# Kernel tuning notes

Measured on AMD Instinct MI355X. Metric: run time of the kernel, lower is better.

## Reference

```python
import jax, jax.numpy as jnp
import numpy as np

B, S, D, K = 32, 512, 512, 2048
NHEADS, NHASH, HLEN = 8, 4, 16
COMMIT = 0.25


def _conv1d(x, w, b):
    # x: [B, C, S], w: [O, I, k] (torch Conv1d layout), 'same' padding for odd k
    k = w.shape[-1]
    y = jax.lax.conv_general_dilated(x, w, (1,), [(k // 2, k // 2)],
                                     dimension_numbers=('NCH', 'OIH', 'NCH'))
    return y + b[None, :, None]


def _mha(x, in_w, in_b, out_w, out_b, nheads):
    # torch nn.MultiheadAttention (batch_first) with packed in_proj
    b, s, d = x.shape
    dh = d // nheads
    qkv = x @ in_w.T + in_b
    q, k, v = jnp.split(qkv, 3, axis=-1)
    sp = lambda t: t.reshape(b, s, nheads, dh).transpose(0, 2, 1, 3)
    q, k, v = sp(q), sp(k), sp(v)
    attn = jax.nn.softmax(jnp.einsum('bhqd,bhkd->bhqk', q, k) * (dh ** -0.5), axis=-1)
    o = jnp.einsum('bhqk,bhkd->bhqd', attn, v).transpose(0, 2, 1, 3).reshape(b, s, d)
    return o @ out_w.T + out_b


def setup_inputs() -> dict:
    key = jax.random.key(0)
    ks = jax.random.split(key, 16)
    w = lambda k, shape, s=0.02: jax.random.normal(k, shape, jnp.float32) * s
    z = lambda *shape: jnp.zeros(shape, jnp.float32)
    return {
        'market_data': jax.random.normal(ks[0], (B, S, D), jnp.float32),
        'W_in': w(ks[1], (D, D)), 'b_in': z(D),
        'pos_enc': w(ks[2], (S, D)),
        'conv3_w': w(ks[3], (D, D, 3)), 'conv3_b': z(D),
        'conv5_w': w(ks[4], (D, D, 5)), 'conv5_b': z(D),
        'conv7_w': w(ks[5], (D, D, 7)), 'conv7_b': z(D),
        'conv9_w': w(ks[6], (D, D, 9)), 'conv9_b': z(D),
        'ms_proj_w': w(ks[7], (D, 4 * D)), 'ms_proj_b': z(D),
        'in_proj_w': w(ks[8], (3 * D, D)), 'in_proj_b': z(3 * D),
        'attn_out_w': w(ks[9], (D, D)), 'attn_out_b': z(D),
        'codebook': jax.random.uniform(ks[10], (K, D), jnp.float32, -1.0 / K, 1.0 / K),
        'hash_w': w(ks[11], (NHASH, HLEN, D), 1.0),
        'reg1_w': w(ks[12], (D // 2, D)), 'reg1_b': z(D // 2),
        'reg2_w': w(ks[13], (K, D // 2)), 'reg2_b': z(K),
    }


def reference(market_data, W_in, b_in, pos_enc, conv3_w, conv3_b, conv5_w, conv5_b,
              conv7_w, conv7_b, conv9_w, conv9_b, ms_proj_w, ms_proj_b,
              in_proj_w, in_proj_b, attn_out_w, attn_out_b, codebook, hash_w,
              reg1_w, reg1_b, reg2_w, reg2_b):
    # input projection
    x = market_data @ W_in.T + b_in                                   # [B,S,D]
    # --- subsequence encoder ---
    xp = x + pos_enc[:x.shape[1]][None]
    xt = xp.transpose(0, 2, 1)                                        # [B,D,S]
    scales = [jax.nn.relu(_conv1d(xt, cw, cb)).transpose(0, 2, 1)
              for cw, cb in ((conv3_w, conv3_b), (conv5_w, conv5_b),
                             (conv7_w, conv7_b), (conv9_w, conv9_b))]
    multi = jnp.concatenate(scales, axis=-1)                          # [B,S,4D]
    proj = multi @ ms_proj_w.T + ms_proj_b                            # [B,S,D]
    enc = proj + _mha(proj, in_proj_w, in_proj_b, attn_out_w, attn_out_b, NHEADS)
    # --- vector quantizer (eval mode: no EMA update) ---
    flat = enc.reshape(-1, D)                                         # [N,D]
    dist = (jnp.sum(flat * flat, axis=1, keepdims=True)
            + jnp.sum(codebook * codebook, axis=1)
            - 2.0 * (flat @ codebook.T))                              # [N,K]
    idx = jnp.argmin(dist, axis=1)                                    # [N]
    quant = codebook[idx].reshape(enc.shape)
    commit = jnp.mean((jax.lax.stop_gradient(quant) - enc) ** 2)
    cb_loss = jnp.mean((quant - jax.lax.stop_gradient(enc)) ** 2)
    vq_loss = COMMIT * commit + cb_loss
    quant_st = enc + jax.lax.stop_gradient(quant - enc)               # straight-through
    # --- hash encoder on semantic ids ---
    hash_codes = (jnp.einsum('bsd,nhd->bsnh', quant_st, hash_w) > 0).astype(jnp.float32)
    # --- regime classifier ---
    h = jax.nn.relu(quant_st @ reg1_w.T + reg1_b)
    regime = jax.nn.softmax(h @ reg2_w.T + reg2_b, axis=-1)
    return (quant_st, vq_loss, idx.reshape(enc.shape[:-1]), hash_codes, regime)
```

## Files before the change

kernel.cpp:

```cpp
#include <hip/hip_runtime.h>
#include <hip/hip_bf16.h>


#define GF_BIAS 1
#define GF_RELU 2
#define GF_ADD  4
#define GF_POS  8
#define GF_ACC  16

typedef _Float16 f16x8 __attribute__((ext_vector_type(8)));
typedef float    f32x4 __attribute__((ext_vector_type(4)));

static constexpr long long O_QUANT = 0LL;
static constexpr long long O_LOSS  = 8388608LL;
static constexpr long long O_IDX   = 8388609LL;
static constexpr long long O_HASH  = 8404993LL;
static constexpr long long O_REG   = 9453569LL;
static constexpr long long O_END   = 43008001LL;

static constexpr long long W_XP    = 0LL;
static constexpr long long W_CT    = 8388608LL;
static constexpr long long W_PROJ  = 16777216LL;
static constexpr long long W_VW    = 25165824LL;
static constexpr long long W_HREG  = 33554432LL;
static constexpr long long W_T     = 34078720LL;
static constexpr long long W_IDX   = 34209792LL;
static constexpr long long W_ASUM  = 34226176LL;
static constexpr long long W_CBB   = 34258944LL;
static constexpr long long W_LPART = 34263040LL;
static constexpr long long W_PBV   = 34271232LL;
static constexpr long long W_PBI   = 34336768LL;
static constexpr long long W_END   = 34402304LL;

__device__ __forceinline__ unsigned int pack_hl(float x)
{
    _Float16 h = (_Float16)x;
    float hf = (float)h;
    _Float16 l = (_Float16)(x - hf);
    unsigned short hb = __builtin_bit_cast(unsigned short, h);
    unsigned short lb = __builtin_bit_cast(unsigned short, l);
    return (unsigned int)hb | ((unsigned int)lb << 16);
}

__device__ __forceinline__ void split2(float x, unsigned short& h, unsigned short& l)
{
    _Float16 hf = (_Float16)x;
    _Float16 lf = (_Float16)(x - (float)hf);
    h = __builtin_bit_cast(unsigned short, hf);
    l = __builtin_bit_cast(unsigned short, lf);
}

__device__ __forceinline__ float unpack_sum(unsigned int u)
{
    _Float16 h = __builtin_bit_cast(_Float16, (unsigned short)(u & 0xffff));
    _Float16 l = __builtin_bit_cast(_Float16, (unsigned short)(u >> 16));
    return (float)h + (float)l;
}

__global__ __launch_bounds__(256)
void split_inplace_r21(float* __restrict__ p)
{
    long long i = (long long)blockIdx.x*256 + threadIdx.x;
    float x = p[i];
    ((unsigned int*)p)[i] = pack_hl(x);
}

__global__ __launch_bounds__(256)
void split_cb_r21(const float* __restrict__ cb, unsigned int* __restrict__ cbhl)
{
    long long i = (long long)blockIdx.x*256 + threadIdx.x;
    cbhl[i] = pack_hl(cb[i] * 2048.0f);
}

template<int KT>
__global__ __launch_bounds__(256)
void conv_w_tr_r21(const float* __restrict__ w, unsigned int* __restrict__ wt)
{
    long long i = (long long)blockIdx.x*256 + threadIdx.x;
    int o  = (int)(i / (512*KT));
    int rem= (int)(i % (512*KT));
    int t  = rem >> 9;
    int ii = rem & 511;
    wt[i] = pack_hl(w[(long long)o*512*KT + (long long)ii*KT + t]);
}

template<int KT>
__global__ __launch_bounds__(256)
void conv_mfma_r21(const unsigned int* __restrict__ xphl,
                   const unsigned int* __restrict__ wthl,
                   const float* __restrict__ bias, float* __restrict__ outp)
{
    constexpr int PAD = KT / 2;
    __shared__ unsigned short Ah[136][40];
    __shared__ unsigned short Al[136][40];
    __shared__ unsigned short Bh[128][40];
    __shared__ unsigned short Bl[128][40];
    const int tid  = threadIdx.x;
    const int lane = tid & 63;
    const int wave = tid >> 6;
    const int wm = (wave >> 1) * 64, wn = (wave & 1) * 64;
    const int bm = blockIdx.x * 128, bn = blockIdx.y * 128;
    const int l15 = lane & 15;
    const int lk8 = (lane >> 4) * 8;
    const int rbase = (lane >> 4) * 4;
    const int sb = bm & 511;
    const int brow0 = tid >> 3, bc = tid & 7;

    f32x4 acc[4][4];
    #pragma unroll
    for (int i=0;i<4;i++)
        #pragma unroll
        for (int j=0;j<4;j++)
            acc[i][j] = (f32x4){0.f,0.f,0.f,0.f};

    for (int i0 = 0; i0 < 512; i0 += 32) {
        __syncthreads();
        for (int sl = tid; sl < 136*8; sl += 256) {
            const int row = sl >> 3, c = sl & 7;
            const int srow = sb + row - 4;
            uint4 v = make_uint4(0u,0u,0u,0u);
            if (srow >= 0 && srow < 512)
                v = *(const uint4*)(xphl + (long long)(bm + row - 4)*512 + i0 + c*4);
            Ah[row][c*4+0] = (unsigned short)(v.x & 0xffff);
            Ah[row][c*4+1] = (unsigned short)(v.y & 0xffff);
            Ah[row][c*4+2] = (unsigned short)(v.z & 0xffff);
            Ah[row][c*4+3] = (unsigned short)(v.w & 0xffff);
            Al[row][c*4+0] = (unsigned short)(v.x >> 16);
            Al[row][c*4+1] = (unsigned short)(v.y >> 16);
            Al[row][c*4+2] = (unsigned short)(v.z >> 16);
            Al[row][c*4+3] = (unsigned short)(v.w >> 16);
        }
        uint4 vb[4];
        #pragma unroll
        for (int q = 0; q < 4; ++q) {
            const int row = brow0 + q*32;
            vb[q] = *(const uint4*)(wthl + (long long)(bn + row)*(KT*512) + 0*512 + i0 + bc*4);
        }
        for (int t = 0; t < KT; ++t) {
            #pragma unroll
            for (int q = 0; q < 4; ++q) {
                const int row = brow0 + q*32;
                Bh[row][bc*4+0] = (unsigned short)(vb[q].x & 0xffff);
                Bh[row][bc*4+1] = (unsigned short)(vb[q].y & 0xffff);
                Bh[row][bc*4+2] = (unsigned short)(vb[q].z & 0xffff);
                Bh[row][bc*4+3] = (unsigned short)(vb[q].w & 0xffff);
                Bl[row][bc*4+0] = (unsigned short)(vb[q].x >> 16);
                Bl[row][bc*4+1] = (unsigned short)(vb[q].y >> 16);
                Bl[row][bc*4+2] = (unsigned short)(vb[q].z >> 16);
                Bl[row][bc*4+3] = (unsigned short)(vb[q].w >> 16);
            }
            if (t + 1 < KT) {
                #pragma unroll
                for (int q = 0; q < 4; ++q) {
                    const int row = brow0 + q*32;
                    vb[q] = *(const uint4*)(wthl + (long long)(bn + row)*(KT*512) + (t+1)*512 + i0 + bc*4);
                }
            }
            __syncthreads();
            const int tofs = t - PAD + 4;
            f16x8 ah[4], al[4], bh[4], bl[4];
            #pragma unroll
            for (int mi = 0; mi < 4; ++mi) {
                ah[mi] = *(const f16x8*)(&Ah[wm + mi*16 + l15 + tofs][lk8]);
                al[mi] = *(const f16x8*)(&Al[wm + mi*16 + l15 + tofs][lk8]);
            }
            #pragma unroll
            for (int nj = 0; nj < 4; ++nj) {
                bh[nj] = *(const f16x8*)(&Bh[wn + nj*16 + l15][lk8]);
                bl[nj] = *(const f16x8*)(&Bl[wn + nj*16 + l15][lk8]);
            }
            #pragma unroll
            for (int mi = 0; mi < 4; ++mi)
                #pragma unroll
                for (int nj = 0; nj < 4; ++nj) {
                    acc[mi][nj] = __builtin_amdgcn_mfma_f32_16x16x32_f16(ah[mi], bh[nj], acc[mi][nj], 0, 0, 0);
                    acc[mi][nj] = __builtin_amdgcn_mfma_f32_16x16x32_f16(ah[mi], bl[nj], acc[mi][nj], 0, 0, 0);
                    acc[mi][nj] = __builtin_amdgcn_mfma_f32_16x16x32_f16(al[mi], bh[nj], acc[mi][nj], 0, 0, 0);
                }
            if (t + 1 < KT) __syncthreads();
        }
    }
    #pragma unroll
    for (int mi = 0; mi < 4; ++mi) {
        #pragma unroll
        for (int nj = 0; nj < 4; ++nj) {
            const int col = bn + wn + nj*16 + l15;
            const float bcol = bias[col];
            #pragma unroll
            for (int r = 0; r < 4; ++r) {
                const int row = bm + wm + mi*16 + rbase + r;
                float v = acc[mi][nj][r] + bcol;
                outp[(long long)row*512 + col] = fmaxf(v, 0.0f);
            }
        }
    }
}

template<int FLAGS>
__global__ __launch_bounds__(256)
void gemm_mfma_r21(const float* __restrict__ A, const float* __restrict__ Bm,
                   const float* __restrict__ bias, const float* __restrict__ pos,
                   const float* __restrict__ addsrc, float* __restrict__ C,
                   int Kdim, int lda, int ldb, int ldc)
{
    __shared__ unsigned short Ah[128][56];
    __shared__ unsigned short Al[128][56];
    __shared__ unsigned short Bh[128][56];
    __shared__ unsigned short Bl[128][56];
    const int tid  = threadIdx.x;
    const int lane = tid & 63;
    const int wave = tid >> 6;
    const int wm = (wave >> 1) * 64, wn = (wave & 1) * 64;
    const int bm = blockIdx.x * 128, bn = blockIdx.y * 128;
    const int l15 = lane & 15;
    const int lk8 = (lane >> 4) * 8;
    const int rbase = (lane >> 4) * 4;
    const int cg   = tid & 7;
    const int rw0  = tid >> 3;

    f32x4 acc[4][4];
    #pragma unroll
    for (int i=0;i<4;i++)
        #pragma unroll
        for (int j=0;j<4;j++)
            acc[i][j] = (f32x4){0.f,0.f,0.f,0.f};

    for (int k0 = 0; k0 < Kdim; k0 += 32) {
        float4 fa[4], fb[4];
        #pragma unroll
        for (int q = 0; q < 4; ++q) {
            const int row = rw0 + q*32;
            fa[q] = *(const float4*)(A  + (long long)(bm + row)*lda + k0 + cg*4);
            fb[q] = *(const float4*)(Bm + (long long)(bn + row)*ldb + k0 + cg*4);
        }
        __syncthreads();
        #pragma unroll
        for (int q = 0; q < 4; ++q) {
            const int row = rw0 + q*32;
            ushort4 ah_, al_, bh_, bl_;
            split2(fa[q].x, ah_.x, al_.x);
            split2(fa[q].y, ah_.y, al_.y);
            split2(fa[q].z, ah_.z, al_.z);
            split2(fa[q].w, ah_.w, al_.w);
            split2(fb[q].x, bh_.x, bl_.x);
            split2(fb[q].y, bh_.y, bl_.y);
            split2(fb[q].z, bh_.z, bl_.z);
            split2(fb[q].w, bh_.w, bl_.w);
            *(ushort4*)(&Ah[row][cg*4]) = ah_;
            *(ushort4*)(&Al[row][cg*4]) = al_;
            *(ushort4*)(&Bh[row][cg*4]) = bh_;
            *(ushort4*)(&Bl[row][cg*4]) = bl_;
        }
        __syncthreads();
        f16x8 ah[4], al[4], bh[4], bl[4];
        #pragma unroll
        for (int mi = 0; mi < 4; ++mi) {
            ah[mi] = *(const f16x8*)(&Ah[wm + mi*16 + l15][lk8]);
            al[mi] = *(const f16x8*)(&Al[wm + mi*16 + l15][lk8]);
        }
        #pragma unroll
        for (int nj = 0; nj < 4; ++nj) {
            bh[nj] = *(const f16x8*)(&Bh[wn + nj*16 + l15][lk8]);
            bl[nj] = *(const f16x8*)(&Bl[wn + nj*16 + l15][lk8]);
        }
        #pragma unroll
        for (int mi = 0; mi < 4; ++mi)
            #pragma unroll
            for (int nj = 0; nj < 4; ++nj) {
                acc[mi][nj] = __builtin_amdgcn_mfma_f32_16x16x32_f16(ah[mi], bh[nj], acc[mi][nj], 0, 0, 0);
                acc[mi][nj] = __builtin_amdgcn_mfma_f32_16x16x32_f16(ah[mi], bl[nj], acc[mi][nj], 0, 0, 0);
                acc[mi][nj] = __builtin_amdgcn_mfma_f32_16x16x32_f16(al[mi], bh[nj], acc[mi][nj], 0, 0, 0);
            }
    }
    #pragma unroll
    for (int mi = 0; mi < 4; ++mi) {
        #pragma unroll
        for (int nj = 0; nj < 4; ++nj) {
            const int col = bn + wn + nj*16 + l15;
            #pragma unroll
            for (int r = 0; r < 4; ++r) {
                const int row = bm + wm + mi*16 + rbase + r;
                float v = acc[mi][nj][r];
                if constexpr (FLAGS & GF_BIAS) v += bias[col];
                if constexpr (FLAGS & GF_POS)  v += pos[(long long)(row & 511)*512 + col];
                if constexpr (FLAGS & GF_ADD)  v += addsrc[(long long)row*ldc + col];
                if constexpr (FLAGS & GF_ACC)  v += C[(long long)row*ldc + col];
                if constexpr (FLAGS & GF_RELU) v = fmaxf(v, 0.0f);
                C[(long long)row*ldc + col] = v;
            }
        }
    }
}

__global__ __launch_bounds__(256)
void attn_mfma_r21(const float* __restrict__ Qbuf, const float* __restrict__ Kbuf,
                   const float* __restrict__ Vbuf, float* __restrict__ att)
{
    __shared__ unsigned short Qh[64][68];
    __shared__ unsigned short Ql[64][68];
    __shared__ unsigned short Kh[64][68];
    __shared__ unsigned short Kl[64][68];
    __shared__ unsigned short Vh[64][68];
    __shared__ unsigned short Vl[64][68];
    const int tid  = threadIdx.x;
    const int lane = tid & 63;
    const int wave = tid >> 6;
    const int l15  = lane & 15;
    const int lq   = lane >> 4;
    const int lq8  = lq * 8;
    const int bid = blockIdx.x;
    const int qt = bid & 7, h = (bid >> 3) & 7, b = bid >> 6;
    const int row0 = b*512 + qt*64;

    #pragma unroll
    for (int u = 0; u < 16; ++u) {
        int e = u*256 + tid;
        int r = e >> 6, c = e & 63;
        float q = Qbuf[(long long)(row0 + r)*512 + h*64 + c] * 0.125f;
        unsigned short hs, ls;
        split2(q, hs, ls);
        Qh[r][c] = hs; Ql[r][c] = ls;
    }

    float m[4], l[4];
    f32x4 accO[4];
    #pragma unroll
    for (int r=0;r<4;r++){ m[r] = -1e30f; l[r] = 0.f; }
    #pragma unroll
    for (int j=0;j<4;j++) accO[j] = (f32x4){0.f,0.f,0.f,0.f};

    for (int kv = 0; kv < 512; kv += 64) {
        __syncthreads();
        #pragma unroll
        for (int u = 0; u < 16; ++u) {
            int e = u*256 + tid;
            int r = e >> 6, c = e & 63;
            float kvf = Kbuf[(long long)(b*512 + kv + r)*512 + h*64 + c];
            float vvf = Vbuf[(long long)(b*512 + kv + r)*512 + h*64 + c];
            unsigned short hs, ls;
            split2(kvf, hs, ls);
            Kh[r][c] = hs; Kl[r][c] = ls;
            split2(vvf, hs, ls);
            Vh[c][r] = hs; Vl[c][r] = ls;
        }
        __syncthreads();
        f32x4 accS[4];
        #pragma unroll
        for (int j=0;j<4;j++) accS[j] = (f32x4){0.f,0.f,0.f,0.f};
        #pragma unroll
        for (int ks = 0; ks < 2; ++ks) {
            f16x8 qh = *(const f16x8*)(&Qh[wave*16 + l15][ks*32 + lq8]);
            f16x8 ql = *(const f16x8*)(&Ql[wave*16 + l15][ks*32 + lq8]);
            #pragma unroll
            for (int nj = 0; nj < 4; ++nj) {
                f16x8 kh = *(const f16x8*)(&Kh[nj*16 + l15][ks*32 + lq8]);
                f16x8 kl = *(const f16x8*)(&Kl[nj*16 + l15][ks*32 + lq8]);
                accS[nj] = __builtin_amdgcn_mfma_f32_16x16x32_f16(qh, kh, accS[nj], 0, 0, 0);
                accS[nj] = __builtin_amdgcn_mfma_f32_16x16x32_f16(qh, kl, accS[nj], 0, 0, 0);
                accS[nj] = __builtin_amdgcn_mfma_f32_16x16x32_f16(ql, kh, accS[nj], 0, 0, 0);
            }
        }
        #pragma unroll
        for (int r = 0; r < 4; ++r) {
            float tm = fmaxf(fmaxf(accS[0][r], accS[1][r]), fmaxf(accS[2][r], accS[3][r]));
            #pragma unroll
            for (int msk = 1; msk < 16; msk <<= 1) tm = fmaxf(tm, __shfl_xor(tm, msk, 64));
            float mn = fmaxf(m[r], tm);
            float scale = expf(m[r] - mn);
            float rs = 0.f;
            #pragma unroll
            for (int nj = 0; nj < 4; ++nj) {
                float p = expf(accS[nj][r] - mn);
                accS[nj][r] = p;
                rs += p;
            }
            #pragma unroll
            for (int msk = 1; msk < 16; msk <<= 1) rs += __shfl_xor(rs, msk, 64);
            l[r] = l[r]*scale + rs;
            m[r] = mn;
            #pragma unroll
            for (int nj = 0; nj < 4; ++nj) accO[nj][r] *= scale;
        }
        __syncthreads();
        #pragma unroll
        for (int r = 0; r < 4; ++r)
            #pragma unroll
            for (int nj = 0; nj < 4; ++nj) {
                unsigned short hs, ls;
                split2(accS[nj][r], hs, ls);
                Kh[wave*16 + lq*4 + r][nj*16 + l15] = hs;
                Kl[wave*16 + lq*4 + r][nj*16 + l15] = ls;
            }
        __syncthreads();
        #pragma unroll
        for (int ks = 0; ks < 2; ++ks) {
            f16x8 ph = *(const f16x8*)(&Kh[wave*16 + l15][ks*32 + lq8]);
            f16x8 pl = *(const f16x8*)(&Kl[wave*16 + l15][ks*32 + lq8]);
            #pragma unroll
            for (int nj = 0; nj < 4; ++nj) {
                f16x8 vh = *(const f16x8*)(&Vh[nj*16 + l15][ks*32 + lq8]);
                f16x8 vl = *(const f16x8*)(&Vl[nj*16 + l15][ks*32 + lq8]);
                accO[nj] = __builtin_amdgcn_mfma_f32_16x16x32_f16(ph, vh, accO[nj], 0, 0, 0);
                accO[nj] = __builtin_amdgcn_mfma_f32_16x16x32_f16(ph, vl, accO[nj], 0, 0, 0);
                accO[nj] = __builtin_amdgcn_mfma_f32_16x16x32_f16(pl, vh, accO[nj], 0, 0, 0);
            }
        }
    }
    #pragma unroll
    for (int nj = 0; nj < 4; ++nj)
        #pragma unroll
        for (int r = 0; r < 4; ++r) {
            const int row = row0 + wave*16 + lq*4 + r;
            att[(long long)row*512 + h*64 + nj*16 + l15] = accO[nj][r] / l[r];
        }
}

__global__ __launch_bounds__(256)
void row_sumsq_r21(const float* __restrict__ X, double* __restrict__ outp)
{
    const int row  = blockIdx.x*4 + (threadIdx.x >> 6);
    const int lane = threadIdx.x & 63;
    double s = 0.0;
    #pragma unroll
    for (int u = 0; u < 8; ++u) {
        float v = X[(long long)row*512 + lane + u*64];
        s += (double)v * (double)v;
    }
    #pragma unroll
    for (int msk = 32; msk; msk >>= 1) s += __shfl_xor(s, msk, 64);
    if (lane == 0) outp[row] = s;
}

__global__ __launch_bounds__(256)
void vq_argmin_mfma_r21(const unsigned int* __restrict__ enchl,
                        const unsigned int* __restrict__ cbhl,
                        const double* __restrict__ Asum, const double* __restrict__ cbB,
                        float* __restrict__ pbv, int* __restrict__ pbi)
{
    __shared__ unsigned int smem[10240];
    unsigned short* AhP = (unsigned short*)smem;
    unsigned short* AlP = AhP + 128*40;
    unsigned short* BhP = AlP + 128*40;
    unsigned short* BlP = BhP + 128*40;
    float* bvsP = (float*)smem;
    int*   bisP = (int*)(smem + 4096);

    const int tid  = threadIdx.x;
    const int lane = tid & 63;
    const int wave = tid >> 6;
    const int wm = (wave >> 1) * 64, wn = (wave & 1) * 64;
    const int bm = blockIdx.x * 128;
    const int l15 = lane & 15;
    const int lk8 = (lane >> 4) * 8;
    const int rbase = (lane >> 4) * 4;
    const int cg   = tid & 7;
    const int rw0  = tid >> 3;

    float bestv[16]; int besti[16];
    #pragma unroll
    for (int g = 0; g < 16; ++g) { bestv[g] = 3.0e38f; besti[g] = 2048; }

    for (int nb = 0; nb < 4; ++nb) {
        const int ct0 = blockIdx.y * 512 + nb * 128;
        f32x4 acc[4][4];
        #pragma unroll
        for (int i=0;i<4;i++)
            #pragma unroll
            for (int j=0;j<4;j++)
                acc[i][j] = (f32x4){0.f,0.f,0.f,0.f};

        for (int k0 = 0; k0 < 512; k0 += 32) {
            uint4 va[4], vb[4];
            #pragma unroll
            for (int q = 0; q < 4; ++q) {
                const int row = rw0 + q*32;
                va[q] = *(const uint4*)(enchl + (long long)(bm + row)*512 + k0 + cg*4);
                vb[q] = *(const uint4*)(cbhl  + (long long)(ct0 + row)*512 + k0 + cg*4);
            }
            __syncthreads();
            #pragma unroll
            for (int q = 0; q < 4; ++q) {
                const int row = rw0 + q*32;
                AhP[row*40 + cg*4+0] = (unsigned short)(va[q].x & 0xffff);
                AhP[row*40 + cg*4+1] = (unsigned short)(va[q].y & 0xffff);
                AhP[row*40 + cg*4+2] = (unsigned short)(va[q].z & 0xffff);
                AhP[row*40 + cg*4+3] = (unsigned short)(va[q].w & 0xffff);
                AlP[row*40 + cg*4+0] = (unsigned short)(va[q].x >> 16);
// ... 25 lines not shown
            for (int mi = 0; mi < 4; ++mi)
                #pragma unroll
                for (int nj = 0; nj < 4; ++nj) {
                    acc[mi][nj] = __builtin_amdgcn_mfma_f32_16x16x32_f16(ah[mi], bh[nj], acc[mi][nj], 0, 0, 0);
                    acc[mi][nj] = __builtin_amdgcn_mfma_f32_16x16x32_f16(ah[mi], bl[nj], acc[mi][nj], 0, 0, 0);
                    acc[mi][nj] = __builtin_amdgcn_mfma_f32_16x16x32_f16(al[mi], bh[nj], acc[mi][nj], 0, 0, 0);
                }
        }
        #pragma unroll
        for (int mi = 0; mi < 4; ++mi) {
            #pragma unroll
            for (int r = 0; r < 4; ++r) {
                const int g = mi*4 + r;
                const float anf = (float)Asum[bm + wm + mi*16 + rbase + r];
                #pragma unroll
                for (int nj = 0; nj < 4; ++nj) {
                    const int col = ct0 + wn + nj*16 + l15;
                    const float bf = (float)cbB[col];
                    const float s1 = anf + bf;
                    const float dot = acc[mi][nj][r] * (1.0f/2048.0f);
                    const float df  = 2.0f * dot;
                    const float qd  = s1 - df;
                    if (qd < bestv[g] || (qd == bestv[g] && col < besti[g])) {
                        bestv[g] = qd; besti[g] = col;
                    }
                }
            }
        }
    }
    __syncthreads();
    #pragma unroll
    for (int mi = 0; mi < 4; ++mi)
        #pragma unroll
        for (int r = 0; r < 4; ++r) {
            const int row  = wm + mi*16 + rbase + r;
            const int slot = (wave & 1)*16 + l15;
            bvsP[row*32 + slot] = bestv[mi*4 + r];
            bisP[row*32 + slot] = besti[mi*4 + r];
        }
    __syncthreads();
    if (tid < 128) {
        float bv = bvsP[tid*32]; int bi = bisP[tid*32];
        #pragma unroll
        for (int s = 1; s < 32; ++s) {
            float v = bvsP[tid*32 + s]; int ii = bisP[tid*32 + s];
            if (v < bv || (v == bv && ii < bi)) { bv = v; bi = ii; }
        }
        pbv[(long long)blockIdx.y*16384 + bm + tid] = bv;
        pbi[(long long)blockIdx.y*16384 + bm + tid] = bi;
    }
}

__global__ __launch_bounds__(256)
void vq_reduce_r21(const float* __restrict__ pbv, const int* __restrict__ pbi,
                   int* __restrict__ idxout, float* __restrict__ out)
{
    int n = blockIdx.x*256 + threadIdx.x;
    if (n >= 16384) return;
    float bv = pbv[n]; int bi = pbi[n];
    #pragma unroll
    for (int q = 1; q < 4; ++q) {
        float v = pbv[q*16384 + n]; int ii = pbi[q*16384 + n];
        if (v < bv || (v == bv && ii < bi)) { bv = v; bi = ii; }
    }
    int ci = bi & 2047;
    idxout[n] = ci;
    out[O_IDX + n] = (float)ci;
}

__global__ __launch_bounds__(256)
void vq_loss_partial_r21(const unsigned int* __restrict__ enchl,
                         const float* __restrict__ cb,
                         const int* __restrict__ idxp, double* __restrict__ part)
{
    __shared__ double red[4];
    const int row  = blockIdx.x*4 + (threadIdx.x >> 6);
    const int lane = threadIdx.x & 63;
    const int ci = idxp[row] & 2047;
    double s = 0.0;
    #pragma unroll
    for (int u = 0; u < 8; ++u) {
        int d = lane + u*64;
        float e = unpack_sum(enchl[(long long)row*512 + d]);
        double dv = (double)cb[(long long)ci*512 + d] - (double)e;
        s += dv * dv;
    }
    #pragma unroll
    for (int msk = 32; msk; msk >>= 1) s += __shfl_xor(s, msk, 64);
    if (lane == 0) red[threadIdx.x >> 6] = s;
    __syncthreads();
    if (threadIdx.x == 0)
        part[blockIdx.x] = red[0] + red[1] + red[2] + red[3];
}

template<int FLAGS>
__global__ __launch_bounds__(256)
void gemm_bt_r21(const float* __restrict__ A, const float* __restrict__ Bm,
                 const float* __restrict__ bias, const float* __restrict__ pos,
                 const float* __restrict__ addsrc, float* __restrict__ C,
                 int Kdim, int lda, int ldb, int ldc)
{
    __shared__ float As[16][132];
    __shared__ float Bs[16][132];
    const int tid = threadIdx.x;
    const int tx = tid & 15, ty = tid >> 4;
    const int bm = blockIdx.x * 128, bn = blockIdx.y * 128;
    const int r0 = tid >> 2;
    const int kg = (tid & 3) << 2;
    const float* Arow0 = A  + (long long)(bm + r0) * lda + kg;
    const float* Arow1 = A  + (long long)(bm + r0 + 64) * lda + kg;
    const float* Brow0 = Bm + (long long)(bn + r0) * ldb + kg;
    const float* Brow1 = Bm + (long long)(bn + r0 + 64) * ldb + kg;

    float acc[8][8] = {};
    for (int k0 = 0; k0 < Kdim; k0 += 16) {
        float4 a0 = *(const float4*)(Arow0 + k0);
        float4 a1 = *(const float4*)(Arow1 + k0);
        float4 b0 = *(const float4*)(Brow0 + k0);
        float4 b1 = *(const float4*)(Brow1 + k0);
        __syncthreads();
        As[kg+0][r0]=a0.x; As[kg+1][r0]=a0.y; As[kg+2][r0]=a0.z; As[kg+3][r0]=a0.w;
        As[kg+0][r0+64]=a1.x; As[kg+1][r0+64]=a1.y; As[kg+2][r0+64]=a1.z; As[kg+3][r0+64]=a1.w;
        Bs[kg+0][r0]=b0.x; Bs[kg+1][r0]=b0.y; Bs[kg+2][r0]=b0.z; Bs[kg+3][r0]=b0.w;
        Bs[kg+0][r0+64]=b1.x; Bs[kg+1][r0+64]=b1.y; Bs[kg+2][r0+64]=b1.z; Bs[kg+3][r0+64]=b1.w;
        __syncthreads();
        #pragma unroll
        for (int kk = 0; kk < 16; ++kk) {
            float a[8], b[8];
            #pragma unroll
            for (int i=0;i<8;i++) a[i] = As[kk][ty*8+i];
            #pragma unroll
            for (int j=0;j<4;j++) b[j]   = Bs[kk][tx*4+j];
            #pragma unroll
            for (int j=0;j<4;j++) b[4+j] = Bs[kk][64+tx*4+j];
            #pragma unroll
            for (int i=0;i<8;i++)
                #pragma unroll
                for (int j=0;j<8;j++)
                    acc[i][j] = fmaf(a[i], b[j], acc[i][j]);
        }
    }
    #pragma unroll
    for (int i=0;i<8;i++){
        const int row = bm + ty*8 + i;
        #pragma unroll
        for (int j=0;j<8;j++){
            const int col = bn + ((j < 4) ? (tx*4 + j) : (64 + tx*4 + (j-4)));
            float v = acc[i][j];
            if constexpr (FLAGS & GF_BIAS) v += bias[col];
            if constexpr (FLAGS & GF_POS)  v += pos[(long long)(row & 511)*512 + col];
            if constexpr (FLAGS & GF_ADD)  v += addsrc[(long long)row*ldc + col];
            if constexpr (FLAGS & GF_ACC)  v += C[(long long)row*ldc + col];
            if constexpr (FLAGS & GF_RELU) v = fmaxf(v, 0.0f);
            C[(long long)row*ldc + col] = v;
        }
    }
}

__global__ __launch_bounds__(256)
void softmax_rows_r21(float* __restrict__ R)
{
    const int row = blockIdx.x;
    const int tid = threadIdx.x;
    __shared__ float  redf[256];
    __shared__ double redd[256];
    float* p = R + (long long)row * 2048;
    float mx = -1e30f;
    for (int c = tid; c < 2048; c += 256) mx = fmaxf(mx, p[c]);
    redf[tid] = mx; __syncthreads();
    for (int s2 = 128; s2; s2 >>= 1) { if (tid < s2) redf[tid] = fmaxf(redf[tid], redf[tid+s2]); __syncthreads(); }
    mx = redf[0];
    double sum = 0.0;
    for (int c = tid; c < 2048; c += 256) { float e = expf(p[c] - mx); p[c] = e; sum += e; }
    redd[tid] = sum; __syncthreads();
    for (int s2 = 128; s2; s2 >>= 1) { if (tid < s2) redd[tid] += redd[tid+s2]; __syncthreads(); }
    double tot = redd[0];
    for (int c = tid; c < 2048; c += 256) p[c] = (float)((double)p[c] / tot);
}

__global__ __launch_bounds__(256)
void hash_table_r21(const float* __restrict__ cb, const float* __restrict__ hw,
                    float* __restrict__ T)
{
    const int k = blockIdx.x*4 + (threadIdx.x >> 6);
    const int j = threadIdx.x & 63;
    double s = 0.0;
    for (int d = 0; d < 512; ++d)
        s += (double)cb[(long long)k*512 + d] * (double)hw[(long long)j*512 + d];
    T[(long long)k*64 + j] = (s > 0.0) ? 1.0f : 0.0f;
}

__global__ void write_loss_r21(const double* __restrict__ part,
                               float* __restrict__ out)
{
    __shared__ double red[256];
    double s = 0.0;
    for (int i = threadIdx.x; i < 4096; i += 256) s += part[i];
    red[threadIdx.x] = s; __syncthreads();
    for (int s2 = 128; s2; s2 >>= 1) {
        if (threadIdx.x < s2) red[threadIdx.x] += red[threadIdx.x + s2];
        __syncthreads();
    }
    if (threadIdx.x == 0)
        out[O_LOSS] = (float)(1.25 * red[0] / 8388608.0);
}

__global__ __launch_bounds__(256)
void write_regime_r21(const float* __restrict__ R, const int* __restrict__ idxp,
                      float* __restrict__ out)
{
    long long i = (long long)blockIdx.x*256 + threadIdx.x;
    if (i >= 33554432LL) return;
    int n = (int)(i >> 11), c = (int)(i & 2047);
    int ci = idxp[n] & 2047;
    out[O_REG + i] = R[(long long)ci*2048 + c];
}

__global__ __launch_bounds__(256)
void write_hash_r21(const float* __restrict__ T, const int* __restrict__ idxp,
                    float* __restrict__ out)
{
    long long i = (long long)blockIdx.x*256 + threadIdx.x;
    if (i >= 1048576LL) return;
    int n = (int)(i >> 6), j = (int)(i & 63);
    int ci = idxp[n] & 2047;
    out[O_HASH + i] = T[(long long)ci*64 + j];
}

__global__ __launch_bounds__(256)
void write_quant_r21(const float* __restrict__ cb, const int* __restrict__ idxp,
                     float* __restrict__ out)
{
    long long i = (long long)blockIdx.x*256 + threadIdx.x;
    if (i >= 8388608LL) return;
    int n = (int)(i >> 9), d = (int)(i & 511);
    int ci = idxp[n] & 2047;
    out[O_QUANT + i] = cb[(long long)ci*512 + d];
}

extern "C" void kernel_launch(void* const* d_in, const int* in_sizes, int n_in,
                              void* d_out, int out_size, void* d_ws, size_t ws_size,
                              hipStream_t stream)
{
    (void)in_sizes; (void)n_in; (void)out_size;
    const float* market = (const float*)d_in[0];
    const float* W_in   = (const float*)d_in[1];
    const float* b_in   = (const float*)d_in[2];
    const float* pos    = (const float*)d_in[3];
    const float* c3w = (const float*)d_in[4];  const float* c3b = (const float*)d_in[5];
    const float* c5w = (const float*)d_in[6];  const float* c5b = (const float*)d_in[7];
    const float* c7w = (const float*)d_in[8];  const float* c7b = (const float*)d_in[9];
    const float* c9w = (const float*)d_in[10]; const float* c9b = (const float*)d_in[11];
    const float* msw = (const float*)d_in[12]; const float* msb = (const float*)d_in[13];
    const float* inw = (const float*)d_in[14]; const float* inb = (const float*)d_in[15];
    const float* aow = (const float*)d_in[16]; const float* aob = (const float*)d_in[17];
    const float* cb  = (const float*)d_in[18]; const float* hw  = (const float*)d_in[19];
    const float* r1w = (const float*)d_in[20]; const float* r1b = (const float*)d_in[21];
    const float* r2w = (const float*)d_in[22]; const float* r2b = (const float*)d_in[23];

    if (ws_size < (size_t)W_END * sizeof(float)) return;

    float* ws    = (float*)d_ws;
    float* xp    = ws + W_XP;
    float* convt = ws + W_CT;
    float* projp = ws + W_PROJ;
    unsigned int* wt3 = (unsigned int*)(ws + W_VW);
    unsigned int* wt5 = wt3 + 512*512*3;
    unsigned int* wt7 = wt5 + 512*512*5;
    unsigned int* wt9 = wt7 + 512*512*7;
    float* Vbufp = ws + W_VW;
    float* hregp = ws + W_HREG;
    float* Tp    = ws + W_T;
    int*    idxp  = (int*)(ws + W_IDX);
    double* asump = (double*)(ws + W_ASUM);
    double* cbbp  = (double*)(ws + W_CBB);
    double* lpart = (double*)(ws + W_LPART);
    float*  pbvp  = ws + W_PBV;
    int*    pbip  = (int*)(ws + W_PBI);
    unsigned int* cbhl = (unsigned int*)(ws + W_PROJ + 4194304);

    float* out = (float*)d_out;

    float* Qbufp = xp;
    float* attp  = xp;
    float* Kbufp = convt;
    float* encp  = convt;
    float* Rp    = projp;

    const unsigned int* xpu  = (const unsigned int*)xp;
    const unsigned int* encu = (const unsigned int*)encp;

    conv_w_tr_r21<3><<<3072, 256, 0, stream>>>(c3w, wt3);
    conv_w_tr_r21<5><<<5120, 256, 0, stream>>>(c5w, wt5);
    conv_w_tr_r21<7><<<7168, 256, 0, stream>>>(c7w, wt7);
    conv_w_tr_r21<9><<<9216, 256, 0, stream>>>(c9w, wt9);

    const dim3 gT(128, 4);

    gemm_mfma_r21<GF_BIAS|GF_POS><<<gT, 256, 0, stream>>>(market, W_in, b_in, pos, nullptr, xp, 512, 512, 512, 512);
    split_inplace_r21<<<32768, 256, 0, stream>>>(xp);

    conv_mfma_r21<3><<<gT, 256, 0, stream>>>(xpu, wt3, c3b, convt);
    gemm_mfma_r21<GF_BIAS><<<gT, 256, 0, stream>>>(convt, msw + 0*512, msb, nullptr, nullptr, projp, 512, 512, 2048, 512);
    conv_mfma_r21<5><<<gT, 256, 0, stream>>>(xpu, wt5, c5b, convt);
    gemm_mfma_r21<GF_ACC><<<gT, 256, 0, stream>>>(convt, msw + 1*512, nullptr, nullptr, nullptr, projp, 512, 512, 2048, 512);
    conv_mfma_r21<7><<<gT, 256, 0, stream>>>(xpu, wt7, c7b, convt);
    gemm_mfma_r21<GF_ACC><<<gT, 256, 0, stream>>>(convt, msw + 2*512, nullptr, nullptr, nullptr, projp, 512, 512, 2048, 512);
    conv_mfma_r21<9><<<gT, 256, 0, stream>>>(xpu, wt9, c9b, convt);
    gemm_mfma_r21<GF_ACC><<<gT, 256, 0, stream>>>(convt, msw + 3*512, nullptr, nullptr, nullptr, projp, 512, 512, 2048, 512);

    gemm_mfma_r21<GF_BIAS><<<gT, 256, 0, stream>>>(projp, inw + 512*512,  inb + 512,  nullptr, nullptr, Kbufp, 512, 512, 512, 512);
    gemm_mfma_r21<GF_BIAS><<<gT, 256, 0, stream>>>(projp, inw + 1024*512, inb + 1024, nullptr, nullptr, Vbufp, 512, 512, 512, 512);
    gemm_mfma_r21<GF_BIAS><<<gT, 256, 0, stream>>>(projp, inw,            inb,        nullptr, nullptr, Qbufp, 512, 512, 512, 512);

    attn_mfma_r21<<<2048, 256, 0, stream>>>(Qbufp, Kbufp, Vbufp, attp);

    gemm_mfma_r21<GF_BIAS|GF_ADD><<<gT, 256, 0, stream>>>(attp, aow, aob, nullptr, projp, encp, 512, 512, 512, 512);

    row_sumsq_r21<<<4096, 256, 0, stream>>>(encp, asump);
    row_sumsq_r21<<<512,  256, 0, stream>>>(cb, cbbp);
    split_inplace_r21<<<32768, 256, 0, stream>>>(encp);
    split_cb_r21<<<4096, 256, 0, stream>>>(cb, cbhl);
    vq_argmin_mfma_r21<<<dim3(128, 4), 256, 0, stream>>>(encu, cbhl, asump, cbbp, pbvp, pbip);
    vq_reduce_r21<<<64, 256, 0, stream>>>(pbvp, pbip, idxp, out);
    vq_loss_partial_r21<<<4096, 256, 0, stream>>>(encu, cb, idxp, lpart);

    gemm_bt_r21<GF_BIAS|GF_RELU><<<dim3(16, 2),  256, 0, stream>>>(cb, r1w, r1b, nullptr, nullptr, hregp, 512, 512, 512, 256);
    gemm_bt_r21<GF_BIAS><<<dim3(16, 16), 256, 0, stream>>>(hregp, r2w, r2b, nullptr, nullptr, Rp, 256, 256, 256, 2048);
    softmax_rows_r21<<<2048, 256, 0, stream>>>(Rp);
    hash_table_r21<<<512, 256, 0, stream>>>(cb, hw, Tp);

    write_loss_r21<<<1, 256, 0, stream>>>(lpart, out);
    write_regime_r21<<<131072, 256, 0, stream>>>(Rp, idxp, out);
    write_hash_r21<<<4096, 256, 0, stream>>>(Tp, idxp, out);
    write_quant_r21<<<32768, 256, 0, stream>>>(cb, idxp, out);
}
```

Before: 1.554 ms.

## Keep activations in packed fp16 hi/lo format across all GEMMs and attention

Every GEMM, conv and attention kernel now reads and writes activations as a packed hi/lo fp16 pair instead of fp32. Weights and inputs are pre-split once, so the per-tile split2 conversion inside the GEMM and attention loaders goes away. The Q scale is folded into the Q projection epilogue, and the separate in-place split passes over xp and enc are dropped. This adds several weight-split launches, and accumulating through packed pairs could change rounding slightly.

```diff
diff --git a/kernel.cpp b/kernel.cpp
--- a/kernel.cpp
+++ b/kernel.cpp
@@ -4,9 +4,10 @@
 
 #define GF_BIAS 1
 #define GF_RELU 2
-#define GF_ADD  4
+#define GF_ADDP 4
 #define GF_POS  8
-#define GF_ACC  16
+#define GF_ACCP 16
+#define GF_QSCALE 32
 
 typedef _Float16 f16x8 __attribute__((ext_vector_type(8)));
 typedef float    f32x4 __attribute__((ext_vector_type(4)));
@@ -58,15 +59,14 @@
 }
 
 __global__ __launch_bounds__(256)
-void split_inplace_r21(float* __restrict__ p)
+void split_hl_r22(const float* __restrict__ src, unsigned int* __restrict__ dst)
 {
     long long i = (long long)blockIdx.x*256 + threadIdx.x;
-    float x = p[i];
-    ((unsigned int*)p)[i] = pack_hl(x);
-}
-
-__global__ __launch_bounds__(256)
-void split_cb_r21(const float* __restrict__ cb, unsigned int* __restrict__ cbhl)
+    dst[i] = pack_hl(src[i]);
+}
+
+__global__ __launch_bounds__(256)
+void split_cb_r22(const float* __restrict__ cb, unsigned int* __restrict__ cbhl)
 {
     long long i = (long long)blockIdx.x*256 + threadIdx.x;
     cbhl[i] = pack_hl(cb[i] * 2048.0f);
@@ -74,7 +74,7 @@
 
 template<int KT>
 __global__ __launch_bounds__(256)
-void conv_w_tr_r21(const float* __restrict__ w, unsigned int* __restrict__ wt)
+void conv_w_tr_r22(const float* __restrict__ w, unsigned int* __restrict__ wt)
 {
     long long i = (long long)blockIdx.x*256 + threadIdx.x;
     int o  = (int)(i / (512*KT));
@@ -86,9 +86,9 @@
 
 template<int KT>
 __global__ __launch_bounds__(256)
-void conv_mfma_r21(const unsigned int* __restrict__ xphl,
+void conv_mfma_r22(const unsigned int* __restrict__ xphl,
                    const unsigned int* __restrict__ wthl,
-                   const float* __restrict__ bias, float* __restrict__ outp)
+                   const float* __restrict__ bias, unsigned int* __restrict__ outp)
 {
     constexpr int PAD = KT / 2;
     __shared__ unsigned short Ah[136][40];
@@ -190,7 +190,7 @@
             for (int r = 0; r < 4; ++r) {
                 const int row = bm + wm + mi*16 + rbase + r;
                 float v = acc[mi][nj][r] + bcol;
-                outp[(long long)row*512 + col] = fmaxf(v, 0.0f);
+                outp[(long long)row*512 + col] = pack_hl(fmaxf(v, 0.0f));
             }
         }
     }
@@ -198,15 +198,15 @@
 
 template<int FLAGS>
 __global__ __launch_bounds__(256)
-void gemm_mfma_r21(const float* __restrict__ A, const float* __restrict__ Bm,
-                   const float* __restrict__ bias, const float* __restrict__ pos,
-                   const float* __restrict__ addsrc, float* __restrict__ C,
-                   int Kdim, int lda, int ldb, int ldc)
-{
-    __shared__ unsigned short Ah[128][56];
-    __shared__ unsigned short Al[128][56];
-    __shared__ unsigned short Bh[128][56];
-    __shared__ unsigned short Bl[128][56];
+void gemm_hl_r22(const unsigned int* __restrict__ A, const unsigned int* __restrict__ Bm,
+                 const float* __restrict__ bias, const float* __restrict__ pos,
+                 const unsigned int* __restrict__ addsrc, unsigned int* __restrict__ C,
+                 int Kdim, int lda, int ldb, int ldc)
+{
+    __shared__ unsigned short Ah[128][40];
+    __shared__ unsigned short Al[128][40];
+    __shared__ unsigned short Bh[128][40];
+    __shared__ unsigned short Bl[128][40];
     const int tid  = threadIdx.x;
     const int lane = tid & 63;
     const int wave = tid >> 6;
@@ -226,30 +226,33 @@
             acc[i][j] = (f32x4){0.f,0.f,0.f,0.f};
 
     for (int k0 = 0; k0 < Kdim; k0 += 32) {
-        float4 fa[4], fb[4];
+        uint4 va[4], vb[4];
         #pragma unroll
         for (int q = 0; q < 4; ++q) {
             const int row = rw0 + q*32;
-            fa[q] = *(const float4*)(A  + (long long)(bm + row)*lda + k0 + cg*4);
-            fb[q] = *(const float4*)(Bm + (long long)(bn + row)*ldb + k0 + cg*4);
+            va[q] = *(const uint4*)(A  + (long long)(bm + row)*lda + k0 + cg*4);
+            vb[q] = *(const uint4*)(Bm + (long long)(bn + row)*ldb + k0 + cg*4);
         }
         __syncthreads();
         #pragma unroll
         for (int q = 0; q < 4; ++q) {
             const int row = rw0 + q*32;
-            ushort4 ah_, al_, bh_, bl_;
-            split2(fa[q].x, ah_.x, al_.x);
-            split2(fa[q].y, ah_.y, al_.y);
-            split2(fa[q].z, ah_.z, al_.z);
-            split2(fa[q].w, ah_.w, al_.w);
-            split2(fb[q].x, bh_.x, bl_.x);
-            split2(fb[q].y, bh_.y, bl_.y);
-            split2(fb[q].z, bh_.z, bl_.z);
-            split2(fb[q].w, bh_.w, bl_.w);
-            *(ushort4*)(&Ah[row][cg*4]) = ah_;
-            *(ushort4*)(&Al[row][cg*4]) = al_;
-            *(ushort4*)(&Bh[row][cg*4]) = bh_;
-            *(ushort4*)(&Bl[row][cg*4]) = bl_;
+            Ah[row][cg*4+0] = (unsigned short)(va[q].x & 0xffff);
+            Ah[row][cg*4+1] = (unsigned short)(va[q].y & 0xffff);
+            Ah[row][cg*4+2] = (unsigned short)(va[q].z & 0xffff);
+            Ah[row][cg*4+3] = (unsigned short)(va[q].w & 0xffff);
+            Al[row][cg*4+0] = (unsigned short)(va[q].x >> 16);
+            Al[row][cg*4+1] = (unsigned short)(va[q].y >> 16);
+            Al[row][cg*4+2] = (unsigned short)(va[q].z >> 16);
+            Al[row][cg*4+3] = (unsigned short)(va[q].w >> 16);
+            Bh[row][cg*4+0] = (unsigned short)(vb[q].x & 0xffff);
+            Bh[row][cg*4+1] = (unsigned short)(vb[q].y & 0xffff);
+            Bh[row][cg*4+2] = (unsigned short)(vb[q].z & 0xffff);
+            Bh[row][cg*4+3] = (unsigned short)(vb[q].w & 0xffff);
+            Bl[row][cg*4+0] = (unsigned short)(vb[q].x >> 16);
+            Bl[row][cg*4+1] = (unsigned short)(vb[q].y >> 16);
+            Bl[row][cg*4+2] = (unsigned short)(vb[q].z >> 16);
+            Bl[row][cg*4+3] = (unsigned short)(vb[q].w >> 16);
         }
         __syncthreads();
         f16x8 ah[4], al[4], bh[4], bl[4];
@@ -283,18 +286,18 @@
                 float v = acc[mi][nj][r];
                 if constexpr (FLAGS & GF_BIAS) v += bias[col];
                 if constexpr (FLAGS & GF_POS)  v += pos[(long long)(row & 511)*512 + col];
-                if constexpr (FLAGS & GF_ADD)  v += addsrc[(long long)row*ldc + col];
-                if constexpr (FLAGS & GF_ACC)  v += C[(long long)row*ldc + col];
-                if constexpr (FLAGS & GF_RELU) v = fmaxf(v, 0.0f);
-                C[(long long)row*ldc + col] = v;
-            }
-        }
-    }
-}
-
-__global__ __launch_bounds__(256)
-void attn_mfma_r21(const float* __restrict__ Qbuf, const float* __restrict__ Kbuf,
-                   const float* __restrict__ Vbuf, float* __restrict__ att)
+                if constexpr (FLAGS & GF_ADDP) v += unpack_sum(addsrc[(long long)row*ldc + col]);
+                if constexpr (FLAGS & GF_ACCP) v += unpack_sum(C[(long long)row*ldc + col]);
+                if constexpr (FLAGS & GF_QSCALE) v *= 0.125f;
+                C[(long long)row*ldc + col] = pack_hl(v);
+            }
+        }
+    }
+}
+
+__global__ __launch_bounds__(256)
+void attn_mfma_r22(const unsigned int* __restrict__ Qbuf, const unsigned int* __restrict__ Kbuf,
+                   const unsigned int* __restrict__ Vbuf, unsigned int* __restrict__ att)
 {
     __shared__ unsigned short Qh[64][68];
     __shared__ unsigned short Ql[64][68];
@@ -316,10 +319,9 @@
     for (int u = 0; u < 16; ++u) {
         int e = u*256 + tid;
         int r = e >> 6, c = e & 63;
-        float q = Qbuf[(long long)(row0 + r)*512 + h*64 + c] * 0.125f;
-        unsigned short hs, ls;
-        split2(q, hs, ls);
-        Qh[r][c] = hs; Ql[r][c] = ls;
+        unsigned int uq = Qbuf[(long long)(row0 + r)*512 + h*64 + c];
+        Qh[r][c] = (unsigned short)(uq & 0xffff);
+        Ql[r][c] = (unsigned short)(uq >> 16);
     }
 
     float m[4], l[4];
@@ -335,13 +337,12 @@
         for (int u = 0; u < 16; ++u) {
             int e = u*256 + tid;
             int r = e >> 6, c = e & 63;
-            float kvf = Kbuf[(long long)(b*512 + kv + r)*512 + h*64 + c];
-            float vvf = Vbuf[(long long)(b*512 + kv + r)*512 + h*64 + c];
-            unsigned short hs, ls;
-            split2(kvf, hs, ls);
-            Kh[r][c] = hs; Kl[r][c] = ls;
-            split2(vvf, hs, ls);
-            Vh[c][r] = hs; Vl[c][r] = ls;
+            unsigned int uk = Kbuf[(long long)(b*512 + kv + r)*512 + h*64 + c];
+            unsigned int uv = Vbuf[(long long)(b*512 + kv + r)*512 + h*64 + c];
+            Kh[r][c] = (unsigned short)(uk & 0xffff);
+            Kl[r][c] = (unsigned short)(uk >> 16);
+            Vh[c][r] = (unsigned short)(uv & 0xffff);
+            Vl[c][r] = (unsigned short)(uv >> 16);
         }
         __syncthreads();
         f32x4 accS[4];
@@ -411,12 +412,12 @@
         #pragma unroll
         for (int r = 0; r < 4; ++r) {
             const int row = row0 + wave*16 + lq*4 + r;
-            att[(long long)row*512 + h*64 + nj*16 + l15] = accO[nj][r] / l[r];
-        }
-}
-
-__global__ __launch_bounds__(256)
-void row_sumsq_r21(const float* __restrict__ X, double* __restrict__ outp)
+            att[(long long)row*512 + h*64 + nj*16 + l15] = pack_hl(accO[nj][r] / l[r]);
+        }
+}
+
+__global__ __launch_bounds__(256)
+void row_sumsq_r22(const float* __restrict__ X, double* __restrict__ outp)
 {
     const int row  = blockIdx.x*4 + (threadIdx.x >> 6);
     const int lane = threadIdx.x & 63;
@@ -432,7 +433,23 @@
 }
 
 __global__ __launch_bounds__(256)
-void vq_argmin_mfma_r21(const unsigned int* __restrict__ enchl,
+void row_sumsq_hl_r22(const unsigned int* __restrict__ X, double* __restrict__ outp)
+{
+    const int row  = blockIdx.x*4 + (threadIdx.x >> 6);
+    const int lane = threadIdx.x & 63;
+    double s = 0.0;
+    #pragma unroll
+    for (int u = 0; u < 8; ++u) {
+        float v = unpack_sum(X[(long long)row*512 + lane + u*64]);
+        s += (double)v * (double)v;
+    }
+    #pragma unroll
+    for (int msk = 32; msk; msk >>= 1) s += __shfl_xor(s, msk, 64);
+    if (lane == 0) outp[row] = s;
+}
+
+__global__ __launch_bounds__(256)
+void vq_argmin_mfma_r22(const unsigned int* __restrict__ enchl,
                         const unsigned int* __restrict__ cbhl,
                         const double* __restrict__ Asum, const double* __restrict__ cbB,
                         float* __restrict__ pbv, int* __restrict__ pbi)
@@ -564,7 +581,7 @@
 }
 
 __global__ __launch_bounds__(256)
-void vq_reduce_r21(const float* __restrict__ pbv, const int* __restrict__ pbi,
+void vq_reduce_r22(const float* __restrict__ pbv, const int* __restrict__ pbi,
                    int* __restrict__ idxout, float* __restrict__ out)
 {
     int n = blockIdx.x*256 + threadIdx.x;
@@ -581,7 +598,7 @@
 }
 
 __global__ __launch_bounds__(256)
-void vq_loss_partial_r21(const unsigned int* __restrict__ enchl,
+void vq_loss_partial_r22(const unsigned int* __restrict__ enchl,
                          const float* __restrict__ cb,
                          const int* __restrict__ idxp, double* __restrict__ part)
 {
@@ -607,7 +624,7 @@
 
 template<int FLAGS>
 __global__ __launch_bounds__(256)
-void gemm_bt_r21(const float* __restrict__ A, const float* __restrict__ Bm,
+void gemm_bt_r22(const float* __restrict__ A, const float* __restrict__ Bm,
                  const float* __restrict__ bias, const float* __restrict__ pos,
                  const float* __restrict__ addsrc, float* __restrict__ C,
                  int Kdim, int lda, int ldb, int ldc)
@@ -660,9 +677,6 @@
             const int col = bn + ((j < 4) ? (tx*4 + j) : (64 + tx*4 + (j-4)));
             float v = acc[i][j];
             if constexpr (FLAGS & GF_BIAS) v += bias[col];
-            if constexpr (FLAGS & GF_POS)  v += pos[(long long)(row & 511)*512 + col];
-            if constexpr (FLAGS & GF_ADD)  v += addsrc[(long long)row*ldc + col];
-            if constexpr (FLAGS & GF_ACC)  v += C[(long long)row*ldc + col];
             if constexpr (FLAGS & GF_RELU) v = fmaxf(v, 0.0f);
             C[(long long)row*ldc + col] = v;
         }
@@ -670,7 +684,7 @@
 }
 
 __global__ __launch_bounds__(256)
-void softmax_rows_r21(float* __restrict__ R)
+void softmax_rows_r22(float* __restrict__ R)
 {
     const int row = blockIdx.x;
     const int tid = threadIdx.x;
@@ -691,7 +705,7 @@
 }
 
 __global__ __launch_bounds__(256)
-void hash_table_r21(const float* __restrict__ cb, const float* __restrict__ hw,
+void hash_table_r22(const float* __restrict__ cb, const float* __restrict__ hw,
                     float* __restrict__ T)
 {
     const int k = blockIdx.x*4 + (threadIdx.x >> 6);
@@ -702,7 +716,7 @@
     T[(long long)k*64 + j] = (s > 0.0) ? 1.0f : 0.0f;
 }
 
-__global__ void write_loss_r21(const double* __restrict__ part,
+__global__ void write_loss_r22(const double* __restrict__ part,
                                float* __restrict__ out)
 {
     __shared__ double red[256];
@@ -718,7 +732,7 @@
 }
 
 __global__ __launch_bounds__(256)
-void write_regime_r21(const float* __restrict__ R, const int* __restrict__ idxp,
+void write_regime_r22(const float* __restrict__ R, const int* __restrict__ idxp,
                       float* __restrict__ out)
 {
     long long i = (long long)blockIdx.x*256 + threadIdx.x;
@@ -729,7 +743,7 @@
 }
 
 __global__ __launch_bounds__(256)
-void write_hash_r21(const float* __restrict__ T, const int* __restrict__ idxp,
+void write_hash_r22(const float* __restrict__ T, const int* __restrict__ idxp,
                     float* __restrict__ out)
 {
     long long i = (long long)blockIdx.x*256 + threadIdx.x;
@@ -740,7 +754,7 @@
 }
 
 __global__ __launch_bounds__(256)
-void write_quant_r21(const float* __restrict__ cb, const int* __restrict__ idxp,
+void write_quant_r22(const float* __restrict__ cb, const int* __restrict__ idxp,
                      float* __restrict__ out)
 {
     long long i = (long long)blockIdx.x*256 + threadIdx.x;
@@ -772,15 +786,22 @@
 
     if (ws_size < (size_t)W_END * sizeof(float)) return;
 
-    float* ws    = (float*)d_ws;
-    float* xp    = ws + W_XP;
-    float* convt = ws + W_CT;
-    float* projp = ws + W_PROJ;
-    unsigned int* wt3 = (unsigned int*)(ws + W_VW);
+    float* ws = (float*)d_ws;
+    unsigned int* xphl   = (unsigned int*)(ws + W_XP);
+    unsigned int* cthl   = (unsigned int*)(ws + W_CT);
+    unsigned int* projhl = (unsigned int*)(ws + W_PROJ);
+    unsigned int* vwbase = (unsigned int*)(ws + W_VW);
+    unsigned int* wt3 = vwbase;
     unsigned int* wt5 = wt3 + 512*512*3;
     unsigned int* wt7 = wt5 + 512*512*5;
     unsigned int* wt9 = wt7 + 512*512*7;
-    float* Vbufp = ws + W_VW;
+    unsigned int* mswhl  = vwbase + 6291456;
+    unsigned int* winhl  = mswhl + 1048576;
+    unsigned int* inwqhl = winhl + 262144;
+    unsigned int* inwkhl = inwqhl + 262144;
+    unsigned int* vhl    = vwbase;
+    unsigned int* inwvhl = (unsigned int*)(ws + W_HREG);
+    unsigned int* aowhl  = inwvhl + 262144;
     float* hregp = ws + W_HREG;
     float* Tp    = ws + W_T;
     int*    idxp  = (int*)(ws + W_IDX);
@@ -790,60 +811,57 @@
     float*  pbvp  = ws + W_PBV;
     int*    pbip  = (int*)(ws + W_PBI);
     unsigned int* cbhl = (unsigned int*)(ws + W_PROJ + 4194304);
+    float* Rp = ws + W_PROJ;
 
     float* out = (float*)d_out;
 
-    float* Qbufp = xp;
-    float* attp  = xp;
-    float* Kbufp = convt;
-    float* encp  = convt;
-    float* Rp    = projp;
-
-    const unsigned int* xpu  = (const unsigned int*)xp;
-    const unsigned int* encu = (const unsigned int*)encp;
-
-    conv_w_tr_r21<3><<<3072, 256, 0, stream>>>(c3w, wt3);
-    conv_w_tr_r21<5><<<5120, 256, 0, stream>>>(c5w, wt5);
-    conv_w_tr_r21<7><<<7168, 256, 0, stream>>>(c7w, wt7);
-    conv_w_tr_r21<9><<<9216, 256, 0, stream>>>(c9w, wt9);
+    conv_w_tr_r22<3><<<3072, 256, 0, stream>>>(c3w, wt3);
+    conv_w_tr_r22<5><<<5120, 256, 0, stream>>>(c5w, wt5);
+    conv_w_tr_r22<7><<<7168, 256, 0, stream>>>(c7w, wt7);
+    conv_w_tr_r22<9><<<9216, 256, 0, stream>>>(c9w, wt9);
+    split_hl_r22<<<32768, 256, 0, stream>>>(market, cthl);
+    split_hl_r22<<<1024,  256, 0, stream>>>(W_in, winhl);
+    split_hl_r22<<<4096,  256, 0, stream>>>(msw, mswhl);
+    split_hl_r22<<<1024,  256, 0, stream>>>(inw,            inwqhl);
+    split_hl_r22<<<1024,  256, 0, stream>>>(inw + 262144,   inwkhl);
+    split_hl_r22<<<1024,  256, 0, stream>>>(inw + 524288,   inwvhl);
+    split_hl_r22<<<1024,  256, 0, stream>>>(aow, aowhl);
 
     const dim3 gT(128, 4);
 
-    gemm_mfma_r21<GF_BIAS|GF_POS><<<gT, 256, 0, stream>>>(market, W_in, b_in, pos, nullptr, xp, 512, 512, 512, 512);
-    split_inplace_r21<<<32768, 256, 0, stream>>>(xp);
-
-    conv_mfma_r21<3><<<gT, 256, 0, stream>>>(xpu, wt3, c3b, convt);
-    gemm_mfma_r21<GF_BIAS><<<gT, 256, 0, stream>>>(convt, msw + 0*512, msb, nullptr, nullptr, projp, 512, 512, 2048, 512);
-    conv_mfma_r21<5><<<gT, 256, 0, stream>>>(xpu, wt5, c5b, convt);
-    gemm_mfma_r21<GF_ACC><<<gT, 256, 0, stream>>>(convt, msw + 1*512, nullptr, nullptr, nullptr, projp, 512, 512, 2048, 512);
-    conv_mfma_r21<7><<<gT, 256, 0, stream>>>(xpu, wt7, c7b, convt);
-    gemm_mfma_r21<GF_ACC><<<gT, 256, 0, stream>>>(convt, msw + 2*512, nullptr, nullptr, nullptr, projp, 512, 512, 2048, 512);
-    conv_mfma_r21<9><<<gT, 256, 0, stream>>>(xpu, wt9, c9b, convt);
-    gemm_mfma_r21<GF_ACC><<<gT, 256, 0, stream>>>(convt, msw + 3*512, nullptr, nullptr, nullptr, projp, 512, 512, 2048, 512);
-
-    gemm_mfma_r21<GF_BIAS><<<gT, 256, 0, stream>>>(projp, inw + 512*512,  inb + 512,  nullptr, nullptr, Kbufp, 512, 512, 512, 512);
-    gemm_mfma_r21<GF_BIAS><<<gT, 256, 0, stream>>>(projp, inw + 1024*512, inb + 1024, nullptr, nullptr, Vbufp, 512, 512, 512, 512);
-    gemm_mfma_r21<GF_BIAS><<<gT, 256, 0, stream>>>(projp, inw,            inb,        nullptr, nullptr, Qbufp, 512, 512, 512, 512);
-
-    attn_mfma_r21<<<2048, 256, 0, stream>>>(Qbufp, Kbufp, Vbufp, attp);
-
-    gemm_mfma_r21<GF_BIAS|GF_ADD><<<gT, 256, 0, stream>>>(attp, aow, aob, nullptr, projp, encp, 512, 512, 512, 512);
-
-    row_sumsq_r21<<<4096, 256, 0, stream>>>(encp, asump);
-    row_sumsq_r21<<<512,  256, 0, stream>>>(cb, cbbp);
-    split_inplace_r21<<<32768, 256, 0, stream>>>(encp);
-    split_cb_r21<<<4096, 256, 0, stream>>>(cb, cbhl);
-    vq_argmin_mfma_r21<<<dim3(128, 4), 256, 0, stream>>>(encu, cbhl, asump, cbbp, pbvp, pbip);
-    vq_reduce_r21<<<64, 256, 0, stream>>>(pbvp, pbip, idxp, out);
-    vq_loss_partial_r21<<<4096, 256, 0, stream>>>(encu, cb, idxp, lpart);
-
-    gemm_bt_r21<GF_BIAS|GF_RELU><<<dim3(16, 2),  256, 0, stream>>>(cb, r1w, r1b, nullptr, nullptr, hregp, 512, 512, 512, 256);
-    gemm_bt_r21<GF_BIAS><<<dim3(16, 16), 256, 0, stream>>>(hregp, r2w, r2b, nullptr, nullptr, Rp, 256, 256, 256, 2048);
-    softmax_rows_r21<<<2048, 256, 0, stream>>>(Rp);
-    hash_table_r21<<<512, 256, 0, stream>>>(cb, hw, Tp);
-
-    write_loss_r21<<<1, 256, 0, stream>>>(lpart, out);
-    write_regime_r21<<<131072, 256, 0, stream>>>(Rp, idxp, out);
-    write_hash_r21<<<4096, 256, 0, stream>>>(Tp, idxp, out);
-    write_quant_r21<<<32768, 256, 0, stream>>>(cb, idxp, out);
-}
+    gemm_hl_r22<GF_BIAS|GF_POS><<<gT, 256, 0, stream>>>(cthl, winhl, b_in, pos, nullptr, xphl, 512, 512, 512, 512);
+
+    conv_mfma_r22<3><<<gT, 256, 0, stream>>>(xphl, wt3, c3b, cthl);
+    gemm_hl_r22<GF_BIAS><<<gT, 256, 0, stream>>>(cthl, mswhl + 0*512, msb, nullptr, nullptr, projhl, 512, 512, 2048, 512);
+    conv_mfma_r22<5><<<gT, 256, 0, stream>>>(xphl, wt5, c5b, cthl);
+    gemm_hl_r22<GF_ACCP><<<gT, 256, 0, stream>>>(cthl, mswhl + 1*512, nullptr, nullptr, nullptr, projhl, 512, 512, 2048, 512);
+    conv_mfma_r22<7><<<gT, 256, 0, stream>>>(xphl, wt7, c7b, cthl);
+    gemm_hl_r22<GF_ACCP><<<gT, 256, 0, stream>>>(cthl, mswhl + 2*512, nullptr, nullptr, nullptr, projhl, 512, 512, 2048, 512);
+    conv_mfma_r22<9><<<gT, 256, 0, stream>>>(xphl, wt9, c9b, cthl);
+    gemm_hl_r22<GF_ACCP><<<gT, 256, 0, stream>>>(cthl, mswhl + 3*512, nullptr, nullptr, nullptr, projhl, 512, 512, 2048, 512);
+
+    gemm_hl_r22<GF_BIAS><<<gT, 256, 0, stream>>>(projhl, inwkhl, inb + 512,  nullptr, nullptr, cthl, 512, 512, 512, 512);
+    gemm_hl_r22<GF_BIAS|GF_QSCALE><<<gT, 256, 0, stream>>>(projhl, inwqhl, inb, nullptr, nullptr, xphl, 512, 512, 512, 512);
+    gemm_hl_r22<GF_BIAS><<<gT, 256, 0, stream>>>(projhl, inwvhl, inb + 1024, nullptr, nullptr, vhl, 512, 512, 512, 512);
+
+    attn_mfma_r22<<<2048, 256, 0, stream>>>(xphl, cthl, vhl, xphl);
+
+    gemm_hl_r22<GF_BIAS|GF_ADDP><<<gT, 256, 0, stream>>>(xphl, aowhl, aob, nullptr, projhl, cthl, 512, 512, 512, 512);
+
+    row_sumsq_hl_r22<<<4096, 256, 0, stream>>>(cthl, asump);
+    row_sumsq_r22<<<512,  256, 0, stream>>>(cb, cbbp);
+    split_cb_r22<<<4096, 256, 0, stream>>>(cb, cbhl);
+    vq_argmin_mfma_r22<<<dim3(128, 4), 256, 0, stream>>>(cthl, cbhl, asump, cbbp, pbvp, pbip);
+    vq_reduce_r22<<<64, 256, 0, stream>>>(pbvp, pbip, idxp, out);
+    vq_loss_partial_r22<<<4096, 256, 0, stream>>>(cthl, cb, idxp, lpart);
+
+    gemm_bt_r22<GF_BIAS|GF_RELU><<<dim3(16, 2),  256, 0, stream>>>(cb, r1w, r1b, nullptr, nullptr, hregp, 512, 512, 512, 256);
+    gemm_bt_r22<GF_BIAS><<<dim3(16, 16), 256, 0, stream>>>(hregp, r2w, r2b, nullptr, nullptr, Rp, 256, 256, 256, 2048);
+    softmax_rows_r22<<<2048, 256, 0, stream>>>(Rp);
+    hash_table_r22<<<512, 256, 0, stream>>>(cb, hw, Tp);
+
+    write_loss_r22<<<1, 256, 0, stream>>>(lpart, out);
+    write_regime_r22<<<131072, 256, 0, stream>>>(Rp, idxp, out);
+    write_hash_r22<<<4096, 256, 0, stream>>>(Tp, idxp, out);
+    write_quant_r22<<<32768, 256, 0, stream>>>(cb, idxp, out);
+}
```

New measurement: 1.521 ms. 2.1% less time.
